# Optimization experiments

Hardware: AMD Instinct MI355X
Metric: run time of the kernel (lower is better)

The kernel has to match this reference:

```python
import jax, jax.numpy as jnp
import numpy as np

B, C, H, W = 16, 256, 64, 64
HID, N, SD, NH, HD, NC = 256, 300, 64, 4, 16, 80


def _conv1x1(x, w, b):
    # x: (B,Cin,H,W), w: (Cout,Cin)
    return jnp.einsum('bchw,oc->bohw', x, w) + b[None, :, None, None]


def _lin(x, w, b):
    return x @ w.T + b


def _ln(x, g, b, eps=1e-5):
    mu = x.mean(-1, keepdims=True)
    var = ((x - mu) ** 2).mean(-1, keepdims=True)
    return (x - mu) / jnp.sqrt(var + eps) * g + b


def setup_inputs() -> dict:
    key = jax.random.key(0)
    ks = jax.random.split(key, 16)
    def w(k, shape, s=0.02):
        return jax.random.normal(k, shape, jnp.float32) * s
    return {
        'x': jax.random.normal(ks[0], (B, C, H, W), jnp.float32),
        'spotlight_sources': w(ks[1], (N, SD)),
        'pos_w': w(ks[2], (HID // 2, 2)), 'pos_b': jnp.zeros((HID // 2,), jnp.float32),
        'fp_w': w(ks[3], (HID, C)), 'fp_b': jnp.zeros((HID,), jnp.float32),
        'bn_g': jnp.ones((HID,), jnp.float32), 'bn_b': jnp.zeros((HID,), jnp.float32),
        'bn_m': jnp.zeros((HID,), jnp.float32), 'bn_v': jnp.ones((HID,), jnp.float32),
        'key_w': w(ks[4], (SD, HID)), 'key_b': jnp.zeros((SD,), jnp.float32),
        'val_w': w(ks[5], (HID, HID)), 'val_b': jnp.zeros((HID,), jnp.float32),
        'ctp_w': w(ks[6], (NC, HID)), 'ctp_b': jnp.zeros((NC,), jnp.float32),
        'bb1_w': w(ks[7], (HID, HID)), 'bb1_b': jnp.zeros((HID,), jnp.float32),
        'bbln_g': jnp.ones((HID,), jnp.float32), 'bbln_b': jnp.zeros((HID,), jnp.float32),
        'bb2_w': w(ks[8], (HID // 2, HID)), 'bb2_b': jnp.zeros((HID // 2,), jnp.float32),
        'bb3_w': w(ks[9], (4, HID // 2)), 'bb3_b': jnp.zeros((4,), jnp.float32),
        'ch1_w': w(ks[10], (HID, HID)), 'ch1_b': jnp.zeros((HID,), jnp.float32),
        'chln_g': jnp.ones((HID,), jnp.float32), 'chln_b': jnp.zeros((HID,), jnp.float32),
        'ch2_w': w(ks[11], (HID // 2, HID)), 'ch2_b': jnp.zeros((HID // 2,), jnp.float32),
        'ch3_w': w(ks[12], (1, HID // 2)), 'ch3_b': jnp.zeros((1,), jnp.float32),
    }


def _forward(x, spotlight_sources, pos_w, pos_b, fp_w, fp_b, bn_g, bn_b, bn_m, bn_v,
             key_w, key_b, val_w, val_b, ctp_w, ctp_b,
             bb1_w, bb1_b, bbln_g, bbln_b, bb2_w, bb2_b, bb3_w, bb3_b,
             ch1_w, ch1_b, chln_g, chln_b, ch2_w, ch2_b, ch3_w, ch3_b):
    Bv, _, Hh, Ww = x.shape
    # position encoding: 2-channel normalized (y, x) grid, conv1x1 to HID//2
    y = jnp.linspace(-1.0, 1.0, Hh, dtype=jnp.float32)
    xc = jnp.linspace(-1.0, 1.0, Ww, dtype=jnp.float32)
    coords = jnp.stack([jnp.broadcast_to(y[:, None], (Hh, Ww)),
                        jnp.broadcast_to(xc[None, :], (Hh, Ww))], 0)[None]  # (1,2,H,W)
    # feature_proj: conv1x1 + BatchNorm(eval) + ReLU
    feats = _conv1x1(x, fp_w, fp_b)
    feats = (feats - bn_m[None, :, None, None]) / jnp.sqrt(bn_v[None, :, None, None] + 1e-5)
    feats = jax.nn.relu(feats * bn_g[None, :, None, None] + bn_b[None, :, None, None])
    pos = jnp.broadcast_to(_conv1x1(coords, pos_w, pos_b), (Bv, HID // 2, Hh, Ww))
    comb = jnp.concatenate([feats[:, :HID // 2], pos], axis=1)  # (B,HID,H,W)
    keys = _conv1x1(comb, key_w, key_b).reshape(Bv, NH, HD, Hh * Ww)   # (B,h,d,M)
    vals = _conv1x1(comb, val_w, val_b).reshape(Bv, HID, Hh * Ww)      # (B,HID,M)
    q = spotlight_sources.reshape(N, NH, HD)                            # (N,h,d)
    logits = jnp.einsum('nhd,bhdm->bhnm', q, keys) / jnp.sqrt(jnp.float32(HD))
    attn = jax.nn.softmax(logits, axis=-1).mean(axis=1)                 # (B,N,M), head-averaged
    maps = attn.reshape(Bv, N, Hh, Ww)
    sf = jnp.einsum('bnm,bcm->bnc', attn, vals)                         # (B,N,HID)
    def head(z, w1, b1, g, bb, w2, b2, w3, b3):
        z = jax.nn.relu(_ln(_lin(z, w1, b1), g, bb))
        z = jax.nn.relu(_lin(z, w2, b2))
        return _lin(z, w3, b3)
    boxes = head(sf, bb1_w, bb1_b, bbln_g, bbln_b, bb2_w, bb2_b, bb3_w, bb3_b)
    scores = jax.nn.sigmoid(head(sf, ch1_w, ch1_b, chln_g, chln_b, ch2_w, ch2_b, ch3_w, ch3_b))
    cls = _lin(sf, ctp_w, ctp_b)
    # diversity loss: mean off-diagonal cosine similarity of attention rows
    an = attn / jnp.maximum(jnp.linalg.norm(attn, axis=2, keepdims=True), 1e-12)
    sim = jnp.einsum('bnm,bkm->bnk', an, an)
    div = (sim.sum() - jnp.einsum('bnn->', sim)) / (N * (N - 1)) * 0.1
    return boxes, scores, cls, maps, div, sf


def reference(x, spotlight_sources, pos_w, pos_b, fp_w, fp_b, bn_g, bn_b, bn_m, bn_v,
              key_w, key_b, val_w, val_b, ctp_w, ctp_b,
              bb1_w, bb1_b, bbln_g, bbln_b, bb2_w, bb2_b, bb3_w, bb3_b,
              ch1_w, ch1_b, chln_g, chln_b, ch2_w, ch2_b, ch3_w, ch3_b):
    return _forward(x, spotlight_sources, pos_w, pos_b, fp_w, fp_b, bn_g, bn_b, bn_m, bn_v,
                    key_w, key_b, val_w, val_b, ctp_w, ctp_b,
                    bb1_w, bb1_b, bbln_g, bbln_b, bb2_w, bb2_b, bb3_w, bb3_b,
                    ch1_w, ch1_b, chln_g, chln_b, ch2_w, ch2_b, ch3_w, ch3_b)
```

## Files before the change

### kernel.cpp

```cpp
#include <hip/hip_runtime.h>
#include <math.h>

#define BB 16
#define CIN 256
#define MM 4096
#define HIDC 256
#define NQ 300
#define NHH 4
#define HDD 16

#define OFF_BOXES  0
#define OFF_SCORES 19200
#define OFF_CLS    24000
#define OFF_MAPS   408000
#define OFF_DIV    20068800
#define OFF_SF     20068801

#define WS_COMB16  0
#define WS_KEYS16  8388608
#define WS_ATTN16  10485760
#define WS_T32     20316160
#define WS_T16     21544960
#define WS_VALW16  22159360
#define WS_SUMS    22192128
#define WS_NORM    22211328
#define WS_ACC     22216128
#define WS_P       22216192

#define HP_SF16   (WS_P + 0)
#define HP_Z1PRE  (WS_P + 614400)
#define HP_Z1_16  (WS_P + 1843200)
#define HP_Z2BB   (WS_P + 2457600)
#define HP_Z2CH   (WS_P + 2764800)
#define HP_HW     (WS_P + 3072000)
#define WS_Q16    (WS_P + 3200000)
#define WS_XT     25426432
#define WS_COMBT  33815040
#define WS_FPW16  42203648
#define WS_KEYW16 42220032

#define HW_BB1 0
#define HW_CH1 65536
#define HW_BB2 131072
#define HW_CH2 163840
#define HW_CTP 196608

typedef short short8 __attribute__((ext_vector_type(8)));
typedef float floatx4 __attribute__((ext_vector_type(4)));

__device__ __forceinline__ unsigned short f2bf(float f){
  unsigned int u = __float_as_uint(f);
  u = (u + 0x7FFFu + ((u >> 16) & 1u)) >> 16;
  return (unsigned short)u;
}
__device__ __forceinline__ float bf1(unsigned short u){
  return __uint_as_float((unsigned int)u << 16);
}

__global__ void zero_kernel(float* p){ p[0] = 0.f; }

__global__ __launch_bounds__(256) void zero4_kernel(float4* __restrict__ p, int n4){
  int i = blockIdx.x * 256 + threadIdx.x;
  if (i < n4) p[i] = make_float4(0.f, 0.f, 0.f, 0.f);
}

__global__ __launch_bounds__(256) void cast4_bf16_kernel(const float* __restrict__ src,
                                                         unsigned short* __restrict__ dst, int n4){
  int i = blockIdx.x * 256 + threadIdx.x;
  if (i < n4){
    float4 v = ((const float4*)src)[i];
    ushort4 u;
    u.x = f2bf(v.x); u.y = f2bf(v.y); u.z = f2bf(v.z); u.w = f2bf(v.w);
    ((ushort4*)dst)[i] = u;
  }
}

__global__ __launch_bounds__(256) void castq_kernel(const float* __restrict__ ss,
                                                    unsigned short* __restrict__ q16){
  int i = blockIdx.x * 256 + threadIdx.x;
  if (i < 320*64)
    q16[i] = (i < NQ*64) ? f2bf(ss[i] * 0.25f) : (unsigned short)0;
}

__global__ __launch_bounds__(256) void cast_w2_kernel(const float* __restrict__ fp_w,
    const float* __restrict__ key_w,
    unsigned short* __restrict__ fpw16, unsigned short* __restrict__ keyw16){
  int i = blockIdx.x * 256 + threadIdx.x;
  if (i < 128*256) fpw16[i] = f2bf(fp_w[i]);
  if (i < 64*256)  keyw16[i] = f2bf(key_w[i]);
}

__global__ __launch_bounds__(256) void cast_heads_kernel(
    const float* __restrict__ val_w, const float* __restrict__ bb1_w,
    const float* __restrict__ ch1_w, const float* __restrict__ bb2_w,
    const float* __restrict__ ch2_w, const float* __restrict__ ctp_w,
    unsigned short* __restrict__ valw16, unsigned short* __restrict__ hw16){
  int i = blockIdx.x * 256 + threadIdx.x;
  int T = gridDim.x * 256;
  for (int j = i; j < 65536; j += T) valw16[j] = f2bf(val_w[j]);
  for (int j = i; j < 65536; j += T) hw16[HW_BB1 + j] = f2bf(bb1_w[j]);
  for (int j = i; j < 65536; j += T) hw16[HW_CH1 + j] = f2bf(ch1_w[j]);
  for (int j = i; j < 32768; j += T) hw16[HW_BB2 + j] = f2bf(bb2_w[j]);
  for (int j = i; j < 32768; j += T) hw16[HW_CH2 + j] = f2bf(ch2_w[j]);
  for (int j = i; j < 20480; j += T) hw16[HW_CTP + j] = f2bf(ctp_w[j]);
}

__global__ __launch_bounds__(256) void pos_fill_kernel(const float* __restrict__ pos_w,
                                                       const float* __restrict__ pos_b,
                                                       unsigned short* __restrict__ comb16){
  int idx = blockIdx.x * 256 + threadIdx.x;
  int c = idx >> 12;
  int m = idx & 4095;
  int row = m >> 6, col = m & 63;
  float y = -1.f + 2.f * (float)row / 63.f;
  float x = -1.f + 2.f * (float)col / 63.f;
  unsigned short v = f2bf(pos_w[c*2] * y + pos_w[c*2+1] * x + pos_b[c]);
  #pragma unroll
  for (int b = 0; b < BB; b++)
    comb16[((size_t)(b*HIDC + 128 + c))*MM + m] = v;
}

__global__ __launch_bounds__(256) void pos_fillT_kernel(const float* __restrict__ pos_w,
                                                        const float* __restrict__ pos_b,
                                                        unsigned short* __restrict__ combT){
  int lin = blockIdx.x * 256 + threadIdx.x;
  int c4 = (lin & 31) * 4;
  int m  = lin >> 5;
  int row = m >> 6, col = m & 63;
  float y = -1.f + 2.f * (float)row / 63.f;
  float x = -1.f + 2.f * (float)col / 63.f;
  ushort4 u;
  u.x = f2bf(pos_w[(c4+0)*2] * y + pos_w[(c4+0)*2+1] * x + pos_b[c4+0]);
  u.y = f2bf(pos_w[(c4+1)*2] * y + pos_w[(c4+1)*2+1] * x + pos_b[c4+1]);
  u.z = f2bf(pos_w[(c4+2)*2] * y + pos_w[(c4+2)*2+1] * x + pos_b[c4+2]);
  u.w = f2bf(pos_w[(c4+3)*2] * y + pos_w[(c4+3)*2+1] * x + pos_b[c4+3]);
  #pragma unroll
  for (int b = 0; b < BB; b++)
    *(ushort4*)&combT[((size_t)b*MM + m)*CIN + 128 + c4] = u;
}

template<bool INF32>
__global__ __launch_bounds__(256) void transpose_kernel(
    const void* __restrict__ in, unsigned short* __restrict__ outp){
  int b = blockIdx.z;
  int m0 = blockIdx.x * 64;
  int r0 = blockIdx.y * 64;
  __shared__ unsigned short lds[64][68];
  int t = threadIdx.x;
  if (INF32){
    const float* ib = (const float*)in + (size_t)b * CIN * MM;
    #pragma unroll
    for (int j = 0; j < 4; j++){
      int lin = j*256 + t;
      int rr = lin >> 4;
      int m4 = (lin & 15) * 4;
      float4 v = *(const float4*)&ib[(size_t)(r0 + rr)*MM + m0 + m4];
      lds[m4+0][rr] = f2bf(v.x);
      lds[m4+1][rr] = f2bf(v.y);
      lds[m4+2][rr] = f2bf(v.z);
      lds[m4+3][rr] = f2bf(v.w);
    }
  } else {
    const unsigned short* ib = (const unsigned short*)in + (size_t)b * CIN * MM;
    #pragma unroll
    for (int j = 0; j < 4; j++){
      int lin = j*256 + t;
      int rr = lin >> 4;
      int m4 = (lin & 15) * 4;
      ushort4 v = *(const ushort4*)&ib[(size_t)(r0 + rr)*MM + m0 + m4];
      lds[m4+0][rr] = v.x; lds[m4+1][rr] = v.y;
      lds[m4+2][rr] = v.z; lds[m4+3][rr] = v.w;
    }
  }
  __syncthreads();
  unsigned short* ob = outp + (size_t)b * MM * CIN;
  #pragma unroll
  for (int j = 0; j < 4; j++){
    int lin = j*256 + t;
    int mm = lin >> 4;
    int c4 = (lin & 15) * 4;
    ushort4 u;
    u.x = lds[mm][c4+0]; u.y = lds[mm][c4+1];
    u.z = lds[mm][c4+2]; u.w = lds[mm][c4+3];
    *(ushort4*)&ob[(size_t)(m0 + mm)*CIN + r0 + c4] = u;
  }
}

__global__ __launch_bounds__(64) void comb_mfma_kernel(
    const unsigned short* __restrict__ fpw16, const unsigned short* __restrict__ xT16,
    const float* __restrict__ fp_b, const float* __restrict__ bn_g,
    const float* __restrict__ bn_b, const float* __restrict__ bn_m,
    const float* __restrict__ bn_v, unsigned short* __restrict__ comb16){
  int b = blockIdx.z;
  const unsigned short* Bb = xT16 + (size_t)b * MM * CIN;
  unsigned short* cb = comb16 + (size_t)b * HIDC * MM;
  int lane = threadIdx.x;
  int r16 = lane & 15;
  int ko  = (lane >> 4) * 8;
  const unsigned short* arow[4];
  const unsigned short* brow[4];
  #pragma unroll
  for (int i = 0; i < 4; i++){
    arow[i] = fpw16 + (size_t)(blockIdx.y*64 + i*16 + r16) * CIN + ko;
    brow[i] = Bb + (size_t)(blockIdx.x*64 + i*16 + r16) * CIN + ko;
  }
  floatx4 acc[4][4];
  #pragma unroll
  for (int i = 0; i < 4; i++)
    #pragma unroll
    for (int j = 0; j < 4; j++)
      acc[i][j] = (floatx4){0.f, 0.f, 0.f, 0.f};
  short8 a[4], bv[4], a2[4], b2[4];
  #pragma unroll
  for (int i = 0; i < 4; i++){
    a[i]  = *(const short8*)(arow[i]);
    bv[i] = *(const short8*)(brow[i]);
  }
  for (int k = 32; k < CIN; k += 32){
    #pragma unroll
    for (int i = 0; i < 4; i++){
      a2[i] = *(const short8*)(arow[i] + k);
      b2[i] = *(const short8*)(brow[i] + k);
    }
    #pragma unroll
    for (int i = 0; i < 4; i++)
      #pragma unroll
      for (int j = 0; j < 4; j++)
        acc[i][j] = __builtin_amdgcn_mfma_f32_16x16x32_bf16(a[i], bv[j], acc[i][j], 0, 0, 0);
    #pragma unroll
    for (int i = 0; i < 4; i++){ a[i] = a2[i]; bv[i] = b2[i]; }
  }
  #pragma unroll
  for (int i = 0; i < 4; i++)
    #pragma unroll
    for (int j = 0; j < 4; j++)
      acc[i][j] = __builtin_amdgcn_mfma_f32_16x16x32_bf16(a[i], bv[j], acc[i][j], 0, 0, 0);
  int cq = lane & 15, rq = (lane >> 4) * 4;
  #pragma unroll
  for (int i = 0; i < 4; i++){
    #pragma unroll
    for (int reg = 0; reg < 4; reg++){
      int rr = blockIdx.y*64 + i*16 + rq + reg;
      float sc  = rsqrtf(bn_v[rr] + 1e-5f);
      float mul = sc * bn_g[rr];
      float ofs = (fp_b[rr] - bn_m[rr]) * mul + bn_b[rr];
      #pragma unroll
      for (int j = 0; j < 4; j++){
        int cc = blockIdx.x*64 + j*16 + cq;
        float v = fmaxf(acc[i][j][reg] * mul + ofs, 0.f);
        cb[(size_t)rr * MM + cc] = f2bf(v);
      }
    }
  }
}


__global__ __launch_bounds__(256) void attn_sums_kernel(
    const unsigned short* __restrict__ q16, const unsigned short* __restrict__ keysT,
    float* __restrict__ sums){
  int b = blockIdx.z, ny = blockIdx.y, mx = blockIdx.x;
  int tid = threadIdx.x, w = tid >> 6, lane = tid & 63;
  int n0 = ny * 64;
  int l15 = lane & 15, qh = lane >> 4;
  int ko = (qh & 1) * 8;
  bool lo = lane < 32;
  const unsigned short* kT = keysT + (size_t)b * MM * 64;
  int mwb = mx*256 + w*64;
  __shared__ unsigned short qlds[64][72];
  __shared__ float spart[4][NHH][64];
  for (int c = tid; c < 512; c += 256){
    int r = c >> 3, d8 = (c & 7) * 8;
    *(short8*)&qlds[r][d8] = *(const short8*)&q16[(size_t)(n0 + r)*64 + d8];
  }
  __syncthreads();
  short8 zz = {0,0,0,0,0,0,0,0};
  #pragma unroll 1
  for (int h = 0; h < NHH; h++){
    short8 a[4];
    #pragma unroll
    for (int i = 0; i < 4; i++)
      a[i] = lo ? *(const short8*)&qlds[i*16 + l15][h*16 + ko] : zz;
    floatx4 sacc[4];
    #pragma unroll
    for (int i = 0; i < 4; i++) sacc[i] = (floatx4){0.f,0.f,0.f,0.f};
    #pragma unroll
    for (int ms = 0; ms < 4; ms++){
      int m = mwb + ms*16 + l15;
      short8 bf = lo ? *(const short8*)&kT[(size_t)m*64 + h*16 + ko] : zz;
      #pragma unroll
      for (int i = 0; i < 4; i++){
        floatx4 l = __builtin_amdgcn_mfma_f32_16x16x32_bf16(a[i], bf,
                        (floatx4){0.f,0.f,0.f,0.f}, 0, 0, 0);
        sacc[i][0] += __expf(l[0]); sacc[i][1] += __expf(l[1]);
        sacc[i][2] += __expf(l[2]); sacc[i][3] += __expf(l[3]);
      }
    }
    #pragma unroll
    for (int i = 0; i < 4; i++)
      #pragma unroll
      for (int reg = 0; reg < 4; reg++){
        float v = sacc[i][reg];
        v += __shfl_xor(v, 1); v += __shfl_xor(v, 2);
        v += __shfl_xor(v, 4); v += __shfl_xor(v, 8);
        if (l15 == 0) spart[w][h][i*16 + (lane >> 4)*4 + reg] = v;
      }
  }
  __syncthreads();
  if (tid < NHH*64){
    int h = tid >> 6, r = tid & 63, n = n0 + r;
    if (n < NQ){
      float v = spart[0][h][r] + spart[1][h][r] + spart[2][h][r] + spart[3][h][r];
      atomicAdd(&sums[((size_t)b*NHH + h)*NQ + n], v);
    }
  }
}

__global__ __launch_bounds__(256) void attn_emit_kernel(
    const unsigned short* __restrict__ q16, const unsigned short* __restrict__ keysT,
    const float* __restrict__ sums, float* __restrict__ maps,
    unsigned short* __restrict__ attn16, float* __restrict__ norms){
  int b = blockIdx.z, ny = blockIdx.y, mx = blockIdx.x;
  int tid = threadIdx.x, w = tid >> 6, lane = tid & 63;
  int n0 = ny * 64;
  int l15 = lane & 15, qh = lane >> 4;
  int ko = (qh & 1) * 8;
  int rq = qh * 4;
  bool lo = lane < 32;
  __shared__ unsigned short qlds[64][72];
  __shared__ __align__(16) float inv_s[NHH][64];
  __shared__ float npart[4][64];
  for (int c = tid; c < 512; c += 256){
    int r = c >> 3, d8 = (c & 7) * 8;
    *(short8*)&qlds[r][d8] = *(const short8*)&q16[(size_t)(n0 + r)*64 + d8];
  }
  if (tid < NHH*64){
    int h = tid >> 6, r = tid & 63, n = n0 + r;
    inv_s[h][r] = (n < NQ) ? 0.25f / sums[((size_t)b*NHH + h)*NQ + n] : 0.f;
  }
  __syncthreads();
  const unsigned short* kT = keysT + (size_t)b * MM * 64;
  int mwb = mx*256 + w*64;
  short8 zz = {0,0,0,0,0,0,0,0};
  floatx4 nacc[4];
  #pragma unroll
  for (int i = 0; i < 4; i++) nacc[i] = (floatx4){0.f,0.f,0.f,0.f};
  float* mb = maps + (size_t)b * NQ * MM;
  unsigned short* ab = attn16 + (size_t)b * NQ * MM;
  #pragma unroll 1
  for (int ms = 0; ms < 4; ms++){
    asm volatile("" ::: "memory");
    int m = mwb + ms*16 + l15;
    floatx4 o[4];
    #pragma unroll
    for (int i = 0; i < 4; i++) o[i] = (floatx4){0.f,0.f,0.f,0.f};
    #pragma unroll
    for (int h = 0; h < NHH; h++){
      short8 bf = lo ? *(const short8*)&kT[(size_t)m*64 + h*16 + ko] : zz;
      #pragma unroll
      for (int i = 0; i < 4; i++){
        short8 a = lo ? *(const short8*)&qlds[i*16 + l15][h*16 + ko] : zz;
        floatx4 l = __builtin_amdgcn_mfma_f32_16x16x32_bf16(a, bf,
                        (floatx4){0.f,0.f,0.f,0.f}, 0, 0, 0);
        floatx4 iv = *(const floatx4*)&inv_s[h][i*16 + rq];
        o[i][0] += __expf(l[0]) * iv[0];
        o[i][1] += __expf(l[1]) * iv[1];
        o[i][2] += __expf(l[2]) * iv[2];
        o[i][3] += __expf(l[3]) * iv[3];
      }
    }
    #pragma unroll
    for (int i = 0; i < 4; i++){
      nacc[i][0] += o[i][0]*o[i][0]; nacc[i][1] += o[i][1]*o[i][1];
      nacc[i][2] += o[i][2]*o[i][2]; nacc[i][3] += o[i][3]*o[i][3];
      #pragma unroll
      for (int reg = 0; reg < 4; reg++){
        int n = n0 + i*16 + rq + reg;
        if (n < NQ){
          mb[(size_t)n*MM + m] = o[i][reg];
          ab[(size_t)n*MM + m] = f2bf(o[i][reg]);
        }
      }
    }
  }
  #pragma unroll
  for (int i = 0; i < 4; i++)
    #pragma unroll
    for (int reg = 0; reg < 4; reg++){
      float v = nacc[i][reg];
      v += __shfl_xor(v, 1); v += __shfl_xor(v, 2);
      v += __shfl_xor(v, 4); v += __shfl_xor(v, 8);
      if (l15 == 0) npart[w][i*16 + rq + reg] = v;
    }
  __syncthreads();
  if (tid < 64){
    int n = n0 + tid;
    if (n < NQ){
      float v = npart[0][tid] + npart[1][tid] + npart[2][tid] + npart[3][tid];
      atomicAdd(&norms[(size_t)b*NQ + n], v);
    }
  }
}

template<bool RELU>
__global__ __launch_bounds__(64) void mfma_nt_kernel(
    const unsigned short* __restrict__ A, size_t sA,
    const unsigned short* __restrict__ B, size_t sB,
    const float* __restrict__ bias,
    float* __restrict__ C, unsigned short* __restrict__ C16,
    size_t sC, int ldc, int Mr, int Nc, int K){
  int bz = blockIdx.z;
  const unsigned short* Ab = A + (size_t)bz * sA;
  const unsigned short* Bb = B + (size_t)bz * sB;
  int lane = threadIdx.x;
  int r16 = lane & 15;
  int ko  = (lane >> 4) * 8;
  const unsigned short* arow[4];
  const unsigned short* brow[4];
  #pragma unroll
  for (int i = 0; i < 4; i++){
    int m = blockIdx.y*64 + i*16 + r16;
    if (m > Mr - 1) m = Mr - 1;
    arow[i] = Ab + (size_t)m * K + ko;
    int n = blockIdx.x*64 + i*16 + r16;
    if (n > Nc - 1) n = Nc - 1;
    brow[i] = Bb + (size_t)n * K + ko;
  }
  floatx4 acc[4][4];
  #pragma unroll
  for (int i = 0; i < 4; i++)
    #pragma unroll
    for (int j = 0; j < 4; j++)
      acc[i][j] = (floatx4){0.f, 0.f, 0.f, 0.f};
  short8 a[4], bv[4], a2[4], b2[4];
  #pragma unroll
  for (int i = 0; i < 4; i++){
    a[i]  = *(const short8*)(arow[i]);
    bv[i] = *(const short8*)(brow[i]);
  }
  for (int k = 32; k < K; k += 32){
    #pragma unroll
    for (int i = 0; i < 4; i++){
      a2[i] = *(const short8*)(arow[i] + k);
      b2[i] = *(const short8*)(brow[i] + k);
    }
    #pragma unroll
    for (int i = 0; i < 4; i++)
      #pragma unroll
      for (int j = 0; j < 4; j++)
        acc[i][j] = __builtin_amdgcn_mfma_f32_16x16x32_bf16(a[i], bv[j], acc[i][j], 0, 0, 0);
    #pragma unroll
    for (int i = 0; i < 4; i++){ a[i] = a2[i]; bv[i] = b2[i]; }
  }
  #pragma unroll
  for (int i = 0; i < 4; i++)
    #pragma unroll
    for (int j = 0; j < 4; j++)
      acc[i][j] = __builtin_amdgcn_mfma_f32_16x16x32_bf16(a[i], bv[j], acc[i][j], 0, 0, 0);
  int cq = lane & 15, rq = (lane >> 4) * 4;
  #pragma unroll
  for (int j = 0; j < 4; j++){
    int cc = blockIdx.x*64 + j*16 + cq;
    if (cc >= Nc) continue;
    float bv_ = bias ? bias[cc] : 0.f;
    #pragma unroll
    for (int i = 0; i < 4; i++){
      int rbase = blockIdx.y*64 + i*16 + rq;
      #pragma unroll
      for (int reg = 0; reg < 4; reg++){
        int rr = rbase + reg;
        if (rr < Mr){
          float v = acc[i][j][reg] + bv_;
          if (RELU) v = fmaxf(v, 0.f);
          size_t o = (size_t)bz * sC + (size_t)rr * ldc + cc;
          if (C)   C[o] = v;
          if (C16) C16[o] = f2bf(v);
        }
      }
    }
  }
}

__global__ __launch_bounds__(64) void mfma_nt_splitk_kernel(
    const unsigned short* __restrict__ A, size_t sA,
    const unsigned short* __restrict__ B, size_t sB,
    float* __restrict__ C, size_t sC, int ldc, int Mr, int K, int kchunk){
  int nks = K / kchunk;
  int bz = blockIdx.z / nks;
  int kz = blockIdx.z % nks;
  const unsigned short* Ab = A + (size_t)bz * sA + (size_t)kz * kchunk;
  const unsigned short* Bb = B + (size_t)bz * sB + (size_t)kz * kchunk;
  int lane = threadIdx.x;
  int r16 = lane & 15;
  int ko  = (lane >> 4) * 8;
  const unsigned short* arow[4];
  const unsigned short* brow[4];
  #pragma unroll
  for (int i = 0; i < 4; i++){
    int m = blockIdx.y*64 + i*16 + r16;
    if (m > Mr - 1) m = Mr - 1;
    arow[i] = Ab + (size_t)m * K + ko;
    int n = blockIdx.x*64 + i*16 + r16;
    brow[i] = Bb + (size_t)n * K + ko;
  }
  floatx4 acc[4][4];
  #pragma unroll
  for (int i = 0; i < 4; i++)
    #pragma unroll
    for (int j = 0; j < 4; j++)
      acc[i][j] = (floatx4){0.f, 0.f, 0.f, 0.f};
  short8 a[4], bv[4], a2[4], b2[4];
  #pragma unroll
  for (int i = 0; i < 4; i++){
    a[i]  = *(const short8*)(arow[i]);
    bv[i] = *(const short8*)(brow[i]);
  }
  for (int k = 32; k < kchunk; k += 32){
    #pragma unroll
    for (int i = 0; i < 4; i++){
      a2[i] = *(const short8*)(arow[i] + k);
      b2[i] = *(const short8*)(brow[i] + k);
    }
    #pragma unroll
    for (int i = 0; i < 4; i++)
      #pragma unroll
      for (int j = 0; j < 4; j++)
        acc[i][j] = __builtin_amdgcn_mfma_f32_16x16x32_bf16(a[i], bv[j], acc[i][j], 0, 0, 0);
    #pragma unroll
    for (int i = 0; i < 4; i++){ a[i] = a2[i]; bv[i] = b2[i]; }
  }
  #pragma unroll
  for (int i = 0; i < 4; i++)
    #pragma unroll
    for (int j = 0; j < 4; j++)
      acc[i][j] = __builtin_amdgcn_mfma_f32_16x16x32_bf16(a[i], bv[j], acc[i][j], 0, 0, 0);
  int cq = lane & 15, rq = (lane >> 4) * 4;
  #pragma unroll
  for (int j = 0; j < 4; j++){
    int cc = blockIdx.x*64 + j*16 + cq;
    #pragma unroll
    for (int i = 0; i < 4; i++){
      int rbase = blockIdx.y*64 + i*16 + rq;
      #pragma unroll
      for (int reg = 0; reg < 4; reg++){
        int rr = rbase + reg;
        if (rr < Mr)
          atomicAdd(&C[(size_t)bz * sC + (size_t)rr * ldc + cc], acc[i][j][reg]);
      }
    }
  }
}

__global__ __launch_bounds__(256) void ln_relu_kernel(const float* __restrict__ zin,
    const float* __restrict__ g, const float* __restrict__ bvec,
    unsigned short* __restrict__ zout){
  int row = blockIdx.x * 4 + (threadIdx.x >> 6);
  int lane = threadIdx.x & 63;
  float4 v = *(const float4*)&zin[(size_t)row * 256 + lane * 4];
  float s = v.x + v.y + v.z + v.w;
  #pragma unroll
  for (int off = 32; off >= 1; off >>= 1) s += __shfl_xor(s, off);
  float mean = s * (1.f/256.f);
  float dx = v.x - mean, dy = v.y - mean, dz = v.z - mean, dw = v.w - mean;
  float sq = dx*dx + dy*dy + dz*dz + dw*dw;
  #pragma unroll
  for (int off = 32; off >= 1; off >>= 1) sq += __shfl_xor(sq, off);
  float inv = rsqrtf(sq * (1.f/256.f) + 1e-5f);
  float4 gv = *(const float4*)&g[lane * 4];
  float4 bb = *(const float4*)&bvec[lane * 4];
  ushort4 u;
  u.x = f2bf(fmaxf(dx*inv*gv.x + bb.x, 0.f));
  u.y = f2bf(fmaxf(dy*inv*gv.y + bb.y, 0.f));
  u.z = f2bf(fmaxf(dz*inv*gv.z + bb.z, 0.f));
  u.w = f2bf(fmaxf(dw*inv*gv.w + bb.w, 0.f));
  *(ushort4*)&zout[(size_t)row * 256 + lane * 4] = u;
}

__global__ __launch_bounds__(256) void head3_kernel(
    const unsigned short* __restrict__ z2bb, const unsigned short* __restrict__ z2ch,
    const float* __restrict__ bb3_w, const float* __restrict__ bb3_b,
    const float* __restrict__ ch3_w, const float* __restrict__ ch3_b,
    float* __restrict__ boxes, float* __restrict__ scores){
  int row = blockIdx.x * 4 + (threadIdx.x >> 6);
  int lane = threadIdx.x & 63;
  float zb0 = bf1(z2bb[(size_t)row*128 + 2*lane]);
  float zb1 = bf1(z2bb[(size_t)row*128 + 2*lane + 1]);
  float zc0 = bf1(z2ch[(size_t)row*128 + 2*lane]);
  float zc1 = bf1(z2ch[(size_t)row*128 + 2*lane + 1]);
  float acc[5];
  #pragma unroll
  for (int o = 0; o < 4; o++)
    acc[o] = bb3_w[o*128 + 2*lane]*zb0 + bb3_w[o*128 + 2*lane + 1]*zb1;
  acc[4] = ch3_w[2*lane]*zc0 + ch3_w[2*lane + 1]*zc1;
  #pragma unroll
  for (int o = 0; o < 5; o++){
    float v = acc[o];
    #pragma unroll
    for (int off = 32; off >= 1; off >>= 1) v += __shfl_xor(v, off);
    acc[o] = v;
  }
  if (lane == 0){
    #pragma unroll
    for (int o = 0; o < 4; o++)
      boxes[(size_t)row*4 + o] = acc[o] + bb3_b[o];
    float sv = acc[4] + ch3_b[0];
    scores[row] = 1.f / (1.f + __expf(-sv));
  }
}

__global__ __launch_bounds__(256) void simdiv_kernel(const unsigned short* __restrict__ attn16,
    const float* __restrict__ norms, float* __restrict__ acc){
  int b = blockIdx.y;
  int m = blockIdx.x * 256 + threadIdx.x;
  __shared__ float inv_s[NQ];
  __shared__ float red[4];
  for (int i = threadIdx.x; i < NQ; i += 256)
    inv_s[i] = 1.f / fmaxf(sqrtf(norms[(size_t)b * NQ + i]), 1e-12f);
  __syncthreads();
  const unsigned short* ab = attn16 + (size_t)b * NQ * MM;
  float S = 0.f;
  for (int n = 0; n < NQ; n++)
    S += bf1(ab[(size_t)n * MM + m]) * inv_s[n];
  float p = S * S;
  #pragma unroll
  for (int off = 32; off >= 1; off >>= 1) p += __shfl_xor(p, off);
  int w = threadIdx.x >> 6, lane = threadIdx.x & 63;
  if (lane == 0) red[w] = p;
  __syncthreads();
  if (threadIdx.x == 0) atomicAdd(acc, red[0] + red[1] + red[2] + red[3]);
}

__global__ void finalize_kernel(const float* __restrict__ acc, float* __restrict__ out_div){
  out_div[0] = (acc[0] - (float)(BB * NQ)) / (float)(NQ * (NQ - 1)) * 0.1f;
}

extern "C" void kernel_launch(void* const* d_in, const int* in_sizes, int n_in,
                              void* d_out, int out_size, void* d_ws, size_t ws_size,
                              hipStream_t stream){
  const float* x      = (const float*)d_in[0];
  const float* ss     = (const float*)d_in[1];
  const float* pos_w  = (const float*)d_in[2];
  const float* pos_b  = (const float*)d_in[3];
  const float* fp_w   = (const float*)d_in[4];
  const float* fp_b   = (const float*)d_in[5];
  const float* bn_g   = (const float*)d_in[6];
  const float* bn_b   = (const float*)d_in[7];
  const float* bn_m   = (const float*)d_in[8];
  const float* bn_v   = (const float*)d_in[9];
  const float* key_w  = (const float*)d_in[10];
  const float* key_b  = (const float*)d_in[11];
  const float* val_w  = (const float*)d_in[12];
  const float* val_b  = (const float*)d_in[13];
  const float* ctp_w  = (const float*)d_in[14];
  const float* ctp_b  = (const float*)d_in[15];
  const float* bb1_w  = (const float*)d_in[16];
  const float* bb1_b  = (const float*)d_in[17];
  const float* bbln_g = (const float*)d_in[18];
  const float* bbln_b = (const float*)d_in[19];
  const float* bb2_w  = (const float*)d_in[20];
  const float* bb2_b  = (const float*)d_in[21];
  const float* bb3_w  = (const float*)d_in[22];
  const float* bb3_b  = (const float*)d_in[23];
  const float* ch1_w  = (const float*)d_in[24];
  const float* ch1_b  = (const float*)d_in[25];
  const float* chln_g = (const float*)d_in[26];
  const float* chln_b = (const float*)d_in[27];
  const float* ch2_w  = (const float*)d_in[28];
  const float* ch2_b  = (const float*)d_in[29];
  const float* ch3_w  = (const float*)d_in[30];
  const float* ch3_b  = (const float*)d_in[31];

  float* out    = (float*)d_out;
  float* boxes  = out + OFF_BOXES;
  float* scores = out + OFF_SCORES;
  float* cls    = out + OFF_CLS;
  float* maps   = out + OFF_MAPS;
  float* divp   = out + OFF_DIV;
  float* sfout  = out + OFF_SF;

  float* ws = (float*)d_ws;
  unsigned short* comb16 = (unsigned short*)(ws + WS_COMB16);
  unsigned short* keysT  = (unsigned short*)(ws + WS_KEYS16);
  unsigned short* attn16 = (unsigned short*)(ws + WS_ATTN16);
  float*          t32    = ws + WS_T32;
  unsigned short* t16    = (unsigned short*)(ws + WS_T16);
  unsigned short* valw16 = (unsigned short*)(ws + WS_VALW16);
  float* sums  = ws + WS_SUMS;
  float* norms = ws + WS_NORM;
  float* dacc  = ws + WS_ACC;
  unsigned short* sf16   = (unsigned short*)(ws + HP_SF16);
  float*          z1pre  = ws + HP_Z1PRE;
  unsigned short* z1_16  = (unsigned short*)(ws + HP_Z1_16);
  unsigned short* z2bb16 = (unsigned short*)(ws + HP_Z2BB);
  unsigned short* z2ch16 = (unsigned short*)(ws + HP_Z2CH);
  unsigned short* hw16   = (unsigned short*)(ws + HP_HW);
  unsigned short* q16    = (unsigned short*)(ws + WS_Q16);
  unsigned short* xT16   = (unsigned short*)(ws + WS_XT);
  unsigned short* combT  = (unsigned short*)(ws + WS_COMBT);
  unsigned short* fpw16  = (unsigned short*)(ws + WS_FPW16);
  unsigned short* keyw16 = (unsigned short*)(ws + WS_KEYW16);

  zero_kernel<<<1, 1, 0, stream>>>(dacc);
  zero4_kernel<<<1200, 256, 0, stream>>>((float4*)t32, 307200);
  zero4_kernel<<<24, 256, 0, stream>>>((float4*)sums, 6000);
  castq_kernel<<<80, 256, 0, stream>>>(ss, q16);
  cast_w2_kernel<<<128, 256, 0, stream>>>(fp_w, key_w, fpw16, keyw16);

  transpose_kernel<true><<<dim3(64,4,16), 256, 0, stream>>>(x, xT16);
  pos_fill_kernel<<<2048, 256, 0, stream>>>(pos_w, pos_b, comb16);
  pos_fillT_kernel<<<512, 256, 0, stream>>>(pos_w, pos_b, combT);
  comb_mfma_kernel<<<dim3(64,2,16), 64, 0, stream>>>(
      fpw16, xT16, fp_b, bn_g, bn_b, bn_m, bn_v, comb16);
  transpose_kernel<false><<<dim3(64,2,16), 256, 0, stream>>>(comb16, combT);
  mfma_nt_kernel<false><<<dim3(1,64,16), 64, 0, stream>>>(
      combT, (size_t)MM*CIN, keyw16, 0, key_b,
      nullptr, keysT, (size_t)MM*64, 64, MM, 64, CIN);

  attn_sums_kernel<<<dim3(16,5,16), 256, 0, stream>>>(q16, keysT, sums);
  attn_emit_kernel<<<dim3(16,5,16), 256, 0, stream>>>(q16, keysT, sums, maps, attn16, norms);

  mfma_nt_splitk_kernel<<<dim3(4,5,BB*4), 64, 0, stream>>>(
      attn16, (size_t)NQ*MM, comb16, (size_t)HIDC*MM,
      t32, (size_t)NQ*HIDC, HIDC, NQ, MM, MM/4);
  cast4_bf16_kernel<<<1200, 256, 0, stream>>>(t32, t16, 307200);
  cast_heads_kernel<<<256, 256, 0, stream>>>(val_w, bb1_w, ch1_w, bb2_w, ch2_w, ctp_w, valw16, hw16);
  mfma_nt_kernel<false><<<dim3(4,5,BB), 64, 0, stream>>>(
      t16, (size_t)NQ*HIDC, valw16, 0, val_b,
      sfout, sf16, (size_t)NQ*HIDC, HIDC, NQ, HIDC, HIDC);

  mfma_nt_kernel<false><<<dim3(4,75,1), 64, 0, stream>>>(
      sf16, 0, hw16 + HW_BB1, 0, bb1_b, z1pre, nullptr, 0, 256, 4800, 256, 256);
  ln_relu_kernel<<<1200, 256, 0, stream>>>(z1pre, bbln_g, bbln_b, z1_16);
  mfma_nt_kernel<true><<<dim3(2,75,1), 64, 0, stream>>>(
      z1_16, 0, hw16 + HW_BB2, 0, bb2_b, nullptr, z2bb16, 0, 128, 4800, 128, 256);
  mfma_nt_kernel<false><<<dim3(4,75,1), 64, 0, stream>>>(
      sf16, 0, hw16 + HW_CH1, 0, ch1_b, z1pre, nullptr, 0, 256, 4800, 256, 256);
  ln_relu_kernel<<<1200, 256, 0, stream>>>(z1pre, chln_g, chln_b, z1_16);
  mfma_nt_kernel<true><<<dim3(2,75,1), 64, 0, stream>>>(
      z1_16, 0, hw16 + HW_CH2, 0, ch2_b, nullptr, z2ch16, 0, 128, 4800, 128, 256);
  head3_kernel<<<1200, 256, 0, stream>>>(z2bb16, z2ch16, bb3_w, bb3_b, ch3_w, ch3_b, boxes, scores);
  mfma_nt_kernel<false><<<dim3(2,75,1), 64, 0, stream>>>(
      sf16, 0, hw16 + HW_CTP, 0, ctp_b, cls, nullptr, 0, 80, 4800, 80, 256);

  simdiv_kernel<<<dim3(16,16), 256, 0, stream>>>(attn16, norms, dacc);
  finalize_kernel<<<1, 1, 0, stream>>>(dacc, divp);
}
```

Measured before the change: 548.1 us.

## Vectorize attention map stores, halve attn tiles, replace split-K atomics with partial sums

The attention emit kernel swaps the MFMA operands so each lane holds 4 consecutive m values, and writes maps and attn16 with float4/ushort4 stores instead of scalar strided stores. The sums kernel does the same swap and reduces across lanes with 2 shuffles instead of 4. Both kernels get half-size m tiles and twice the grid. The split-K GEMM now writes per-slice partials with plain stores into a reused workspace region, and a new kernel sums the 4 partials while casting to bf16. This removes atomics and the zeroing pass but adds extra partial-buffer traffic. pos_fill is also vectorized to 4-wide stores, one (b,c) row segment per thread.

Measured after the change: 514.1 us. -6.2%, faster.

```diff
diff --git a/kernel.cpp b/kernel.cpp
--- a/kernel.cpp
+++ b/kernel.cpp
@@ -64,11 +64,21 @@
   if (i < n4) p[i] = make_float4(0.f, 0.f, 0.f, 0.f);
 }
 
-__global__ __launch_bounds__(256) void cast4_bf16_kernel(const float* __restrict__ src,
-                                                         unsigned short* __restrict__ dst, int n4){
+__global__ __launch_bounds__(256) void cast_sum4_kernel(const float* __restrict__ part,
+                                                        unsigned short* __restrict__ dst, int n4){
   int i = blockIdx.x * 256 + threadIdx.x;
   if (i < n4){
-    float4 v = ((const float4*)src)[i];
+    int b = i / 19200, r = i - b * 19200;
+    const float4* p0 = (const float4*)part + (size_t)(b*4 + 0) * 19200 + r;
+    const float4* p1 = (const float4*)part + (size_t)(b*4 + 1) * 19200 + r;
+    const float4* p2 = (const float4*)part + (size_t)(b*4 + 2) * 19200 + r;
+    const float4* p3 = (const float4*)part + (size_t)(b*4 + 3) * 19200 + r;
+    float4 a = *p0, bq = *p1, c = *p2, d = *p3;
+    float4 v;
+    v.x = a.x + bq.x + c.x + d.x;
+    v.y = a.y + bq.y + c.y + d.y;
+    v.z = a.z + bq.z + c.z + d.z;
+    v.w = a.w + bq.w + c.w + d.w;
     ushort4 u;
     u.x = f2bf(v.x); u.y = f2bf(v.y); u.z = f2bf(v.z); u.w = f2bf(v.w);
     ((ushort4*)dst)[i] = u;
@@ -108,16 +118,20 @@
 __global__ __launch_bounds__(256) void pos_fill_kernel(const float* __restrict__ pos_w,
                                                        const float* __restrict__ pos_b,
                                                        unsigned short* __restrict__ comb16){
-  int idx = blockIdx.x * 256 + threadIdx.x;
-  int c = idx >> 12;
-  int m = idx & 4095;
+  int lin = blockIdx.x * 256 + threadIdx.x;
+  int m  = (lin & 1023) * 4;
+  int c  = (lin >> 10) & 127;
+  int b  = lin >> 17;
   int row = m >> 6, col = m & 63;
-  float y = -1.f + 2.f * (float)row / 63.f;
-  float x = -1.f + 2.f * (float)col / 63.f;
-  unsigned short v = f2bf(pos_w[c*2] * y + pos_w[c*2+1] * x + pos_b[c]);
-  #pragma unroll
-  for (int b = 0; b < BB; b++)
-    comb16[((size_t)(b*HIDC + 128 + c))*MM + m] = v;
+  float y  = -1.f + 2.f * (float)row / 63.f;
+  float wy = pos_w[c*2], wx = pos_w[c*2+1], pb = pos_b[c];
+  float base = wy * y + pb;
+  ushort4 u;
+  u.x = f2bf(base + wx * (-1.f + 2.f * (float)(col+0) / 63.f));
+  u.y = f2bf(base + wx * (-1.f + 2.f * (float)(col+1) / 63.f));
+  u.z = f2bf(base + wx * (-1.f + 2.f * (float)(col+2) / 63.f));
+  u.w = f2bf(base + wx * (-1.f + 2.f * (float)(col+3) / 63.f));
+  *(ushort4*)&comb16[((size_t)(b*HIDC + 128 + c))*MM + m] = u;
 }
 
 __global__ __launch_bounds__(256) void pos_fillT_kernel(const float* __restrict__ pos_w,
@@ -265,7 +279,7 @@
   int ko = (qh & 1) * 8;
   bool lo = lane < 32;
   const unsigned short* kT = keysT + (size_t)b * MM * 64;
-  int mwb = mx*256 + w*64;
+  int mwb = mx*128 + w*32;
   __shared__ unsigned short qlds[64][72];
   __shared__ float spart[4][NHH][64];
   for (int c = tid; c < 512; c += 256){
@@ -276,34 +290,28 @@
   short8 zz = {0,0,0,0,0,0,0,0};
   #pragma unroll 1
   for (int h = 0; h < NHH; h++){
-    short8 a[4];
-    #pragma unroll
-    for (int i = 0; i < 4; i++)
-      a[i] = lo ? *(const short8*)&qlds[i*16 + l15][h*16 + ko] : zz;
-    floatx4 sacc[4];
-    #pragma unroll
-    for (int i = 0; i < 4; i++) sacc[i] = (floatx4){0.f,0.f,0.f,0.f};
-    #pragma unroll
-    for (int ms = 0; ms < 4; ms++){
+    short8 bq[4];
+    #pragma unroll
+    for (int ni = 0; ni < 4; ni++)
+      bq[ni] = lo ? *(const short8*)&qlds[ni*16 + l15][h*16 + ko] : zz;
+    float sacc[4] = {0.f, 0.f, 0.f, 0.f};
+    #pragma unroll
+    for (int ms = 0; ms < 2; ms++){
       int m = mwb + ms*16 + l15;
-      short8 bf = lo ? *(const short8*)&kT[(size_t)m*64 + h*16 + ko] : zz;
+      short8 a = lo ? *(const short8*)&kT[(size_t)m*64 + h*16 + ko] : zz;
       #pragma unroll
-      for (int i = 0; i < 4; i++){
-        floatx4 l = __builtin_amdgcn_mfma_f32_16x16x32_bf16(a[i], bf,
+      for (int ni = 0; ni < 4; ni++){
+        floatx4 l = __builtin_amdgcn_mfma_f32_16x16x32_bf16(a, bq[ni],
                         (floatx4){0.f,0.f,0.f,0.f}, 0, 0, 0);
-        sacc[i][0] += __expf(l[0]); sacc[i][1] += __expf(l[1]);
-        sacc[i][2] += __expf(l[2]); sacc[i][3] += __expf(l[3]);
+        sacc[ni] += __expf(l[0]) + __expf(l[1]) + __expf(l[2]) + __expf(l[3]);
       }
     }
     #pragma unroll
-    for (int i = 0; i < 4; i++)
-      #pragma unroll
-      for (int reg = 0; reg < 4; reg++){
-        float v = sacc[i][reg];
-        v += __shfl_xor(v, 1); v += __shfl_xor(v, 2);
-        v += __shfl_xor(v, 4); v += __shfl_xor(v, 8);
-        if (l15 == 0) spart[w][h][i*16 + (lane >> 4)*4 + reg] = v;
-      }
+    for (int ni = 0; ni < 4; ni++){
+      float v = sacc[ni];
+      v += __shfl_xor(v, 16); v += __shfl_xor(v, 32);
+      if (lane < 16) spart[w][h][ni*16 + lane] = v;
+    }
   }
   __syncthreads();
   if (tid < NHH*64){
@@ -324,10 +332,9 @@
   int n0 = ny * 64;
   int l15 = lane & 15, qh = lane >> 4;
   int ko = (qh & 1) * 8;
-  int rq = qh * 4;
   bool lo = lane < 32;
   __shared__ unsigned short qlds[64][72];
-  __shared__ __align__(16) float inv_s[NHH][64];
+  __shared__ float inv_s[NHH][64];
   __shared__ float npart[4][64];
   for (int c = tid; c < 512; c += 256){
     int r = c >> 3, d8 = (c & 7) * 8;
@@ -339,58 +346,55 @@
   }
   __syncthreads();
   const unsigned short* kT = keysT + (size_t)b * MM * 64;
-  int mwb = mx*256 + w*64;
+  int mwb = mx*128 + w*32;
   short8 zz = {0,0,0,0,0,0,0,0};
-  floatx4 nacc[4];
-  #pragma unroll
-  for (int i = 0; i < 4; i++) nacc[i] = (floatx4){0.f,0.f,0.f,0.f};
+  float nacc[4] = {0.f, 0.f, 0.f, 0.f};
   float* mb = maps + (size_t)b * NQ * MM;
   unsigned short* ab = attn16 + (size_t)b * NQ * MM;
   #pragma unroll 1
-  for (int ms = 0; ms < 4; ms++){
+  for (int ms = 0; ms < 2; ms++){
     asm volatile("" ::: "memory");
-    int m = mwb + ms*16 + l15;
+    int mbase = mwb + ms*16;
+    int mk = mbase + l15;
     floatx4 o[4];
     #pragma unroll
-    for (int i = 0; i < 4; i++) o[i] = (floatx4){0.f,0.f,0.f,0.f};
+    for (int ni = 0; ni < 4; ni++) o[ni] = (floatx4){0.f,0.f,0.f,0.f};
     #pragma unroll
     for (int h = 0; h < NHH; h++){
-      short8 bf = lo ? *(const short8*)&kT[(size_t)m*64 + h*16 + ko] : zz;
+      short8 a = lo ? *(const short8*)&kT[(size_t)mk*64 + h*16 + ko] : zz;
       #pragma unroll
-      for (int i = 0; i < 4; i++){
-        short8 a = lo ? *(const short8*)&qlds[i*16 + l15][h*16 + ko] : zz;
-        floatx4 l = __builtin_amdgcn_mfma_f32_16x16x32_bf16(a, bf,
+      for (int ni = 0; ni < 4; ni++){
+        short8 bq = lo ? *(const short8*)&qlds[ni*16 + l15][h*16 + ko] : zz;
+        floatx4 l = __builtin_amdgcn_mfma_f32_16x16x32_bf16(a, bq,
                         (floatx4){0.f,0.f,0.f,0.f}, 0, 0, 0);
-        floatx4 iv = *(const floatx4*)&inv_s[h][i*16 + rq];
-        o[i][0] += __expf(l[0]) * iv[0];
-        o[i][1] += __expf(l[1]) * iv[1];
-        o[i][2] += __expf(l[2]) * iv[2];
-        o[i][3] += __expf(l[3]) * iv[3];
+        float iv = inv_s[h][ni*16 + l15];
+        o[ni][0] += __expf(l[0]) * iv;
+        o[ni][1] += __expf(l[1]) * iv;
+        o[ni][2] += __expf(l[2]) * iv;
+        o[ni][3] += __expf(l[3]) * iv;
       }
     }
     #pragma unroll
-    for (int i = 0; i < 4; i++){
-      nacc[i][0] += o[i][0]*o[i][0]; nacc[i][1] += o[i][1]*o[i][1];
-      nacc[i][2] += o[i][2]*o[i][2]; nacc[i][3] += o[i][3]*o[i][3];
-      #pragma unroll
-      for (int reg = 0; reg < 4; reg++){
-        int n = n0 + i*16 + rq + reg;
-        if (n < NQ){
-          mb[(size_t)n*MM + m] = o[i][reg];
-          ab[(size_t)n*MM + m] = f2bf(o[i][reg]);
-        }
+    for (int ni = 0; ni < 4; ni++){
+      nacc[ni] += o[ni][0]*o[ni][0] + o[ni][1]*o[ni][1]
+                + o[ni][2]*o[ni][2] + o[ni][3]*o[ni][3];
+      int n = n0 + ni*16 + l15;
+      if (n < NQ){
+        size_t off = (size_t)n*MM + mbase + qh*4;
+        float4 v; v.x = o[ni][0]; v.y = o[ni][1]; v.z = o[ni][2]; v.w = o[ni][3];
+        *(float4*)&mb[off] = v;
+        ushort4 u;
+        u.x = f2bf(v.x); u.y = f2bf(v.y); u.z = f2bf(v.z); u.w = f2bf(v.w);
+        *(ushort4*)&ab[off] = u;
       }
     }
   }
   #pragma unroll
-  for (int i = 0; i < 4; i++)
-    #pragma unroll
-    for (int reg = 0; reg < 4; reg++){
-      float v = nacc[i][reg];
-      v += __shfl_xor(v, 1); v += __shfl_xor(v, 2);
-      v += __shfl_xor(v, 4); v += __shfl_xor(v, 8);
-      if (l15 == 0) npart[w][i*16 + rq + reg] = v;
-    }
+  for (int ni = 0; ni < 4; ni++){
+    float v = nacc[ni];
+    v += __shfl_xor(v, 16); v += __shfl_xor(v, 32);
+    if (lane < 16) npart[w][ni*16 + lane] = v;
+  }
   __syncthreads();
   if (tid < 64){
     int n = n0 + tid;
@@ -544,7 +548,7 @@
       for (int reg = 0; reg < 4; reg++){
         int rr = rbase + reg;
         if (rr < Mr)
-          atomicAdd(&C[(size_t)bz * sC + (size_t)rr * ldc + cc], acc[i][j][reg]);
+          C[(size_t)blockIdx.z * sC + (size_t)rr * ldc + cc] = acc[i][j][reg];
       }
     }
   }
@@ -681,7 +685,6 @@
   unsigned short* comb16 = (unsigned short*)(ws + WS_COMB16);
   unsigned short* keysT  = (unsigned short*)(ws + WS_KEYS16);
   unsigned short* attn16 = (unsigned short*)(ws + WS_ATTN16);
-  float*          t32    = ws + WS_T32;
   unsigned short* t16    = (unsigned short*)(ws + WS_T16);
   unsigned short* valw16 = (unsigned short*)(ws + WS_VALW16);
   float* sums  = ws + WS_SUMS;
@@ -695,18 +698,18 @@
   unsigned short* hw16   = (unsigned short*)(ws + HP_HW);
   unsigned short* q16    = (unsigned short*)(ws + WS_Q16);
   unsigned short* xT16   = (unsigned short*)(ws + WS_XT);
+  float*          tpart  = ws + WS_XT;
   unsigned short* combT  = (unsigned short*)(ws + WS_COMBT);
   unsigned short* fpw16  = (unsigned short*)(ws + WS_FPW16);
   unsigned short* keyw16 = (unsigned short*)(ws + WS_KEYW16);
 
   zero_kernel<<<1, 1, 0, stream>>>(dacc);
-  zero4_kernel<<<1200, 256, 0, stream>>>((float4*)t32, 307200);
   zero4_kernel<<<24, 256, 0, stream>>>((float4*)sums, 6000);
   castq_kernel<<<80, 256, 0, stream>>>(ss, q16);
   cast_w2_kernel<<<128, 256, 0, stream>>>(fp_w, key_w, fpw16, keyw16);
 
   transpose_kernel<true><<<dim3(64,4,16), 256, 0, stream>>>(x, xT16);
-  pos_fill_kernel<<<2048, 256, 0, stream>>>(pos_w, pos_b, comb16);
+  pos_fill_kernel<<<8192, 256, 0, stream>>>(pos_w, pos_b, comb16);
   pos_fillT_kernel<<<512, 256, 0, stream>>>(pos_w, pos_b, combT);
   comb_mfma_kernel<<<dim3(64,2,16), 64, 0, stream>>>(
       fpw16, xT16, fp_b, bn_g, bn_b, bn_m, bn_v, comb16);
@@ -715,13 +718,13 @@
       combT, (size_t)MM*CIN, keyw16, 0, key_b,
       nullptr, keysT, (size_t)MM*64, 64, MM, 64, CIN);
 
-  attn_sums_kernel<<<dim3(16,5,16), 256, 0, stream>>>(q16, keysT, sums);
-  attn_emit_kernel<<<dim3(16,5,16), 256, 0, stream>>>(q16, keysT, sums, maps, attn16, norms);
+  attn_sums_kernel<<<dim3(32,5,16), 256, 0, stream>>>(q16, keysT, sums);
+  attn_emit_kernel<<<dim3(32,5,16), 256, 0, stream>>>(q16, keysT, sums, maps, attn16, norms);
 
   mfma_nt_splitk_kernel<<<dim3(4,5,BB*4), 64, 0, stream>>>(
       attn16, (size_t)NQ*MM, comb16, (size_t)HIDC*MM,
-      t32, (size_t)NQ*HIDC, HIDC, NQ, MM, MM/4);
-  cast4_bf16_kernel<<<1200, 256, 0, stream>>>(t32, t16, 307200);
+      tpart, (size_t)NQ*HIDC, HIDC, NQ, MM, MM/4);
+  cast_sum4_kernel<<<1200, 256, 0, stream>>>(tpart, t16, 307200);
   cast_heads_kernel<<<256, 256, 0, stream>>>(val_w, bb1_w, ch1_w, bb2_w, ch2_w, ctp_w, valw16, hw16);
   mfma_nt_kernel<false><<<dim3(4,5,BB), 64, 0, stream>>>(
       t16, (size_t)NQ*HIDC, valw16, 0, val_b,
```
